# Kernel tuning notes

Hardware: AMD Instinct MI355X
Metric: run time of the kernel (lower is better)

Reference implementation:

```python
import jax, jax.numpy as jnp
import numpy as np

HEADS = 8
HEAD_DIM = 64
INNER = HEADS * HEAD_DIM  # 512
DIM = 512
B, H, W = 8, 32, 32
KV_LEN, KV_DIM = 77, 1024


def group_norm(x, g, b, groups=32, eps=1e-6):
    # x: [B, C, H, W]
    Bx, C, Hx, Wx = x.shape
    xr = x.reshape(Bx, groups, C // groups, Hx, Wx)
    mu = xr.mean(axis=(2, 3, 4), keepdims=True)
    var = xr.var(axis=(2, 3, 4), keepdims=True)
    xr = (xr - mu) * jax.lax.rsqrt(var + eps)
    return xr.reshape(Bx, C, Hx, Wx) * g[None, :, None, None] + b[None, :, None, None]


def layer_norm(x, g, b, eps=1e-5):
    mu = x.mean(axis=-1, keepdims=True)
    var = x.var(axis=-1, keepdims=True)
    return (x - mu) * jax.lax.rsqrt(var + eps) * g + b


def attention(qx, kvx, Wq, Wk, Wv, Wo, bo):
    # qx: [B, Sq, dim_q], kvx: [B, Sk, dim_kv]
    q = qx @ Wq
    k = kvx @ Wk
    v = kvx @ Wv
    Bx, Sq, _ = q.shape
    Sk = k.shape[1]
    q = q.reshape(Bx, Sq, HEADS, HEAD_DIM)
    k = k.reshape(Bx, Sk, HEADS, HEAD_DIM)
    v = v.reshape(Bx, Sk, HEADS, HEAD_DIM)
    att = jnp.einsum('bqhd,bkhd->bhqk', q, k) * (HEAD_DIM ** -0.5)
    att = jax.nn.softmax(att.astype(jnp.float32), axis=-1).astype(q.dtype)
    o = jnp.einsum('bhqk,bkhd->bqhd', att, v).reshape(Bx, Sq, INNER)
    return o @ Wo + bo


def setup_inputs() -> dict:
    key = jax.random.key(0)
    ks = jax.random.split(key, 20)
    s = 0.02
    def n(k, shape):
        return jax.random.normal(k, shape, jnp.float32) * s
    return {
        'q': jax.random.normal(ks[0], (B, DIM, H, W), jnp.float32),
        'kv': jax.random.normal(ks[1], (B, KV_LEN, KV_DIM), jnp.float32),
        'gn_g': jnp.ones((DIM,), jnp.float32), 'gn_b': jnp.zeros((DIM,), jnp.float32),
        'ln2_g': jnp.ones((INNER,), jnp.float32), 'ln2_b': jnp.zeros((INNER,), jnp.float32),
        'ln3_g': jnp.ones((INNER,), jnp.float32), 'ln3_b': jnp.zeros((INNER,), jnp.float32),
        'ln4_g': jnp.ones((INNER,), jnp.float32), 'ln4_b': jnp.zeros((INNER,), jnp.float32),
        'fc_in_w': n(ks[2], (DIM, INNER)), 'fc_in_b': jnp.zeros((INNER,), jnp.float32),
        'fc_out_w': n(ks[3], (INNER, DIM)), 'fc_out_b': jnp.zeros((DIM,), jnp.float32),
        'a1_q': n(ks[4], (INNER, INNER)), 'a1_k': n(ks[5], (INNER, INNER)),
        'a1_v': n(ks[6], (INNER, INNER)), 'a1_o': n(ks[7], (INNER, INNER)),
        'a1_ob': jnp.zeros((INNER,), jnp.float32),
        'a2_q': n(ks[8], (INNER, INNER)), 'a2_k': n(ks[9], (KV_DIM, INNER)),
        'a2_v': n(ks[10], (KV_DIM, INNER)), 'a2_o': n(ks[11], (INNER, INNER)),
        'a2_ob': jnp.zeros((INNER,), jnp.float32),
        'ff_proj_w': n(ks[12], (INNER, INNER * 8)), 'ff_proj_b': jnp.zeros((INNER * 8,), jnp.float32),
        'ff_out_w': n(ks[13], (INNER * 4, INNER)), 'ff_out_b': jnp.zeros((INNER,), jnp.float32),
    }


def reference(q, kv, gn_g, gn_b, ln2_g, ln2_b, ln3_g, ln3_b, ln4_g, ln4_b,
              fc_in_w, fc_in_b, fc_out_w, fc_out_b,
              a1_q, a1_k, a1_v, a1_o, a1_ob,
              a2_q, a2_k, a2_v, a2_o, a2_ob,
              ff_proj_w, ff_proj_b, ff_out_w, ff_out_b):
    res = q
    Bx, C, Hx, Wx = q.shape
    x = group_norm(q, gn_g, gn_b)
    x = x.reshape(Bx, C, Hx * Wx).transpose(0, 2, 1)  # [B, S, C]
    x = x @ fc_in_w + fc_in_b
    t = layer_norm(x, ln2_g, ln2_b)
    x = attention(t, t, a1_q, a1_k, a1_v, a1_o, a1_ob) + x
    x = attention(layer_norm(x, ln3_g, ln3_b), kv, a2_q, a2_k, a2_v, a2_o, a2_ob) + x
    h = layer_norm(x, ln4_g, ln4_b) @ ff_proj_w + ff_proj_b
    a, gate = jnp.split(h, 2, axis=-1)
    x = (a * jax.nn.gelu(gate, approximate=False)) @ ff_out_w + ff_out_b + x
    x = x @ fc_out_w + fc_out_b
    x = x.transpose(0, 2, 1).reshape(Bx, C, Hx, Wx)
    return x + res
```

## Files before the change

### kernel.cpp

```cpp
#include <hip/hip_runtime.h>
#include <cstdint>
#include <cstddef>

typedef __attribute__((ext_vector_type(8))) short bf16x8;
typedef __attribute__((ext_vector_type(4))) short short4v;
typedef __attribute__((ext_vector_type(4))) float f32x4;

__device__ __forceinline__ short f2b(float f) {
    unsigned u = __builtin_bit_cast(unsigned, f);
    u = (u + 0x7FFFu + ((u >> 16) & 1u)) >> 16;
    return (short)u;
}
__device__ __forceinline__ float b2f(short s) {
    unsigned u = ((unsigned)(unsigned short)s) << 16;
    return __builtin_bit_cast(float, u);
}

__device__ __forceinline__ void gload16(const short* g, short* l) {
    __builtin_amdgcn_global_load_lds(
        (const __attribute__((address_space(1))) unsigned int*)g,
        (__attribute__((address_space(3))) unsigned int*)l, 16, 0, 0);
}

__device__ __forceinline__ float gelu_fast(float g) {
    float g2 = g * g;
    float gp = g * (0.7978845608f + 0.0356774081f * g2);
    float e = exp2f(2.885390082f * gp);
    float th = 1.f - 2.f / (e + 1.f);
    return 0.5f * g * (1.f + th);
}

__device__ __forceinline__ int pn_ffp(int n) {
    int m = (n < 2048) ? n : (n - 2048);
    int gofs = (n < 2048) ? 0 : 32;
    int x = m >> 6, c = m & 63;
    return x * 128 + ((c >> 5) << 6) + gofs + (c & 31);
}

struct PrepArgs {
    const float* src[12];
    short* dst[12];
    const float* kv;
    short* kvb;
    const float* fb;
    float* bp;
};

__global__ __launch_bounds__(256) void prep(PrepArgs a) {
    int t = blockIdx.x;
    int tid = threadIdx.x;
    if (t >= 6144) {
        if (t >= 6452) {
            int n = (t - 6452) * 256 + tid;
            if (n < 4096) a.bp[pn_ffp(n)] = a.fb[n];
            return;
        }
        int idx = (t - 6144) * 256 + tid;
        if (idx >= 78848) return;
        const float4* s = (const float4*)a.kv + (size_t)idx * 2;
        float4 va = s[0], vb = s[1];
        bf16x8 w;
        w[0] = f2b(va.x); w[1] = f2b(va.y); w[2] = f2b(va.z); w[3] = f2b(va.w);
        w[4] = f2b(vb.x); w[5] = f2b(vb.y); w[6] = f2b(vb.z); w[7] = f2b(vb.w);
        *(bf16x8*)(a.kvb + (size_t)idx * 8) = w;
        return;
    }
    const int jstart[12] = {0, 256, 512, 768, 1024, 1280, 1536, 1792, 2304, 2816, 3072, 5120};
    const int jK[12] = {512, 512, 512, 512, 512, 512, 512, 1024, 1024, 512, 512, 2048};
    const int jN[12] = {512, 512, 512, 512, 512, 512, 512, 512, 512, 512, 4096, 512};
    int j = 11;
#pragma unroll
    for (int i = 11; i >= 1; --i)
        if (t < jstart[i]) j = i - 1;
    int tx = t - jstart[j];
    int K = jK[j], N = jN[j];
    int tn = N >> 5;
    int n0 = (tx % tn) * 32, k0 = (tx / tn) * 32;
    const float* w = a.src[j];
    short* wt = a.dst[j];
    bool perm = (j == 10);

    __shared__ float tile[32][33];
    int cx = tid & 31, ty0 = tid >> 5;
#pragma unroll
    for (int i = 0; i < 4; ++i) {
        int r = ty0 + i * 8;
        tile[r][cx] = w[(size_t)(k0 + r) * N + n0 + cx];
    }
    __syncthreads();
    int r = tid >> 3;
    int kg = (tid & 7) * 4;
    int drow = perm ? pn_ffp(n0 + r) : (n0 + r);
    short4v o = {f2b(tile[kg][r]), f2b(tile[kg + 1][r]),
                 f2b(tile[kg + 2][r]), f2b(tile[kg + 3][r])};
    *(short4v*)&wt[(size_t)drow * K + k0 + kg] = o;
}

__global__ __launch_bounds__(256) void gn_stats(const float* __restrict__ q,
                                                const float* __restrict__ g,
                                                const float* __restrict__ bta,
                                                float* __restrict__ sc,
                                                float* __restrict__ sh) {
    int bb = blockIdx.x >> 5, gg = blockIdx.x & 31;
    const float4* src = (const float4*)(q + ((size_t)(bb * 512 + gg * 16)) * 1024);
    float s = 0.f, s2 = 0.f;
#pragma unroll
    for (int i = 0; i < 16; ++i) {
        float4 v = src[threadIdx.x + 256 * i];
        s += (v.x + v.y) + (v.z + v.w);
        s2 += (v.x * v.x + v.y * v.y) + (v.z * v.z + v.w * v.w);
    }
#pragma unroll
    for (int m = 1; m < 64; m <<= 1) {
        s += __shfl_xor(s, m);
        s2 += __shfl_xor(s2, m);
    }
    __shared__ float red[8];
    int wv = threadIdx.x >> 6;
    if ((threadIdx.x & 63) == 0) { red[wv] = s; red[4 + wv] = s2; }
    __syncthreads();
    if (threadIdx.x < 16) {
        float S = red[0] + red[1] + red[2] + red[3];
        float S2 = red[4] + red[5] + red[6] + red[7];
        float mu = S * (1.f / 16384.f);
        float var = S2 * (1.f / 16384.f) - mu * mu;
        float rs = rsqrtf(var + 1e-6f);
        int c = gg * 16 + threadIdx.x;
        float scale = rs * g[c];
        sc[bb * 512 + c] = scale;
        sh[bb * 512 + c] = bta[c] - mu * scale;
    }
}

__global__ __launch_bounds__(256) void gn_apply(const float* __restrict__ q,
                                                const float* __restrict__ sc,
                                                const float* __restrict__ sh,
                                                short* __restrict__ out) {
    __shared__ short tile[512][33];
    int b = blockIdx.x >> 5, st = blockIdx.x & 31;
    int s0 = st * 32;
    int sl = threadIdx.x & 31, cg = threadIdx.x >> 5;
    for (int c = cg; c < 512; c += 8) {
        float v = q[((size_t)(b * 512 + c)) * 1024 + s0 + sl];
        float y = v * sc[b * 512 + c] + sh[b * 512 + c];
        tile[c][sl] = f2b(y);
    }
    __syncthreads();
    int sr = threadIdx.x >> 3, ch = threadIdx.x & 7;
    short* orow = out + ((size_t)(b * 1024 + s0 + sr)) * 512;
    for (int c8 = ch * 64; c8 < ch * 64 + 64; c8 += 8) {
        bf16x8 o;
#pragma unroll
        for (int jj = 0; jj < 8; ++jj) o[jj] = tile[c8 + jj][sr];
        *(bf16x8*)&orow[c8] = o;
    }
}

__global__ __launch_bounds__(256) void ln_rows(const short* __restrict__ x,
                                               const float* __restrict__ g,
                                               const float* __restrict__ bta,
                                               short* __restrict__ out) {
    int row = blockIdx.x * 4 + (threadIdx.x >> 6);
    int lane = threadIdx.x & 63;
    bf16x8 v8 = *(const bf16x8*)(x + (size_t)row * 512 + lane * 8);
    float v[8];
#pragma unroll
    for (int j = 0; j < 8; ++j) v[j] = b2f(v8[j]);
    float s = 0.f, s2 = 0.f;
#pragma unroll
    for (int j = 0; j < 8; ++j) { s += v[j]; s2 += v[j] * v[j]; }
#pragma unroll
    for (int m = 1; m < 64; m <<= 1) {
        s += __shfl_xor(s, m);
        s2 += __shfl_xor(s2, m);
    }
    float mu = s * (1.f / 512.f);
    float var = s2 * (1.f / 512.f) - mu * mu;
    float rs = rsqrtf(var + 1e-5f);
    float4 ga = ((const float4*)g)[lane * 2], gb = ((const float4*)g)[lane * 2 + 1];
    float4 ba = ((const float4*)bta)[lane * 2], bb = ((const float4*)bta)[lane * 2 + 1];
    bf16x8 o;
    o[0] = f2b((v[0] - mu) * rs * ga.x + ba.x);
    o[1] = f2b((v[1] - mu) * rs * ga.y + ba.y);
    o[2] = f2b((v[2] - mu) * rs * ga.z + ba.z);
    o[3] = f2b((v[3] - mu) * rs * ga.w + ba.w);
    o[4] = f2b((v[4] - mu) * rs * gb.x + bb.x);
    o[5] = f2b((v[5] - mu) * rs * gb.y + bb.y);
    o[6] = f2b((v[6] - mu) * rs * gb.z + bb.z);
    o[7] = f2b((v[7] - mu) * rs * gb.w + bb.w);
    *(bf16x8*)(out + (size_t)row * 512 + lane * 8) = o;
}

template <int BN>
__global__ __launch_bounds__(256, 1) void gemm_gl(
    const short* __restrict__ A, const short* __restrict__ BT,
    int M, int N, int K,
    const float* __restrict__ bias,
    const short* __restrict__ addSrcB,
    short* __restrict__ outB,
    const float* __restrict__ resid,
    float* __restrict__ outFinal,
    int mode) {
    constexpr int FJ = BN / 32;
    constexpr int ASZ = 3 * 128 * 32;
    constexpr int BSZ = 3 * BN * 32;
    __shared__ __attribute__((aligned(16))) short smem[ASZ + BSZ];
    short* Asb = smem;
    short* Bsb = smem + ASZ;
    int tid = threadIdx.x;
    int wave = tid >> 6, lane = tid & 63;
    int wr = wave >> 1, wc = wave & 1;
    int m0 = blockIdx.y * 128, n0 = blockIdx.x * BN;
    f32x4 acc[4][FJ];
#pragma unroll
    for (int i = 0; i < 4; ++i)
#pragma unroll
        for (int j = 0; j < FJ; ++j) acc[i][j] = (f32x4){0.f, 0.f, 0.f, 0.f};

    int srow = tid >> 2;
    int scg = (((tid & 3) ^ ((tid >> 3) & 3)) << 3);
    int ar0 = m0 + srow; if (ar0 >= M) ar0 = M - 1;
    int ar1 = m0 + 64 + srow; if (ar1 >= M) ar1 = M - 1;
    const short* ag0 = A + (size_t)ar0 * K + scg;
    const short* ag1 = A + (size_t)ar1 * K + scg;
    const short* bg0 = BT + (size_t)(n0 + srow) * K + scg;
    const short* bg1 = BT + (size_t)(n0 + 64 + srow) * K + scg;
    int nk = K >> 5;

    auto stage = [&](int buf) {
        gload16(ag0, &Asb[buf * 4096 + wave * 512]);
        gload16(ag1, &Asb[buf * 4096 + 2048 + wave * 512]);
        gload16(bg0, &Bsb[buf * (BN * 32) + wave * 512]);
        if constexpr (BN == 128) gload16(bg1, &Bsb[buf * 4096 + 2048 + wave * 512]);
        ag0 += 32; ag1 += 32; bg0 += 32; bg1 += 32;
    };
    stage(0);
    stage(1);

    int lr = lane & 15, g = lane >> 4;
    int cur = 0;
    for (int kt = 0; kt < nk; ++kt) {
        __builtin_amdgcn_sched_barrier(0);
        if (kt + 1 < nk) {
            if constexpr (BN == 128) asm volatile("s_waitcnt vmcnt(4)" ::: "memory");
            else asm volatile("s_waitcnt vmcnt(3)" ::: "memory");
        } else {
            asm volatile("s_waitcnt vmcnt(0)" ::: "memory");
        }
        __builtin_amdgcn_sched_barrier(0);
        __builtin_amdgcn_s_barrier();
        int n2 = cur + 2; if (n2 >= 3) n2 -= 3;
        if (kt + 2 < nk) stage(n2);
        bf16x8 af[4], bfr[FJ];
#pragma unroll
        for (int i = 0; i < 4; ++i) {
            int row = wr * 64 + i * 16 + lr;
            af[i] = *(const bf16x8*)&Asb[cur * 4096 + row * 32 + ((g ^ ((row >> 1) & 3)) << 3)];
        }
#pragma unroll
        for (int j = 0; j < FJ; ++j) {
            int row = wc * (BN / 2) + j * 16 + lr;
            bfr[j] = *(const bf16x8*)&Bsb[cur * (BN * 32) + row * 32 + ((g ^ ((row >> 1) & 3)) << 3)];
        }
#pragma unroll
        for (int i = 0; i < 4; ++i)
#pragma unroll
            for (int j = 0; j < FJ; ++j)
                acc[i][j] = __builtin_amdgcn_mfma_f32_16x16x32_bf16(af[i], bfr[j], acc[i][j], 0, 0, 0);
        cur = cur + 1; if (cur >= 3) cur -= 3;
    }

    int lq = lane >> 4;
    if (mode == 1) {
#pragma unroll
        for (int i = 0; i < 4; ++i)
#pragma unroll
            for (int j = 0; j < FJ; ++j) {
                int mm0 = m0 + wr * 64 + i * 16 + lq * 4;
                int nn = n0 + wc * (BN / 2) + j * 16 + lr;
                int bb = mm0 >> 10, ss = mm0 & 1023;
                size_t oi = ((size_t)(bb * 512 + nn)) * 1024 + ss;
                float bv = bias ? bias[nn] : 0.f;
                float4 rv = *(const float4*)&resid[oi];
                float4 ov;
                ov.x = acc[i][j][0] + bv + rv.x;
                ov.y = acc[i][j][1] + bv + rv.y;
                ov.z = acc[i][j][2] + bv + rv.z;
                ov.w = acc[i][j][3] + bv + rv.w;
                *(float4*)&outFinal[oi] = ov;
            }
        return;
    }
    {
        constexpr int EC = BN + 4;
        float* ef = (float*)smem;
#pragma unroll
        for (int h = 0; h < 2; ++h) {
            __syncthreads();
            if (wr == h) {
#pragma unroll
                for (int i = 0; i < 4; ++i)
#pragma unroll
                    for (int j = 0; j < FJ; ++j)
#pragma unroll
                        for (int r = 0; r < 4; ++r)
                            ef[(i * 16 + lq * 4 + r) * EC + wc * (BN / 2) + j * 16 + lr] =
                                acc[i][j][r];
            }
            __syncthreads();
#pragma unroll
            for (int q = 0; q < BN / 16; ++q) {
                int idx = q * 256 + tid;
                int row = idx / (BN / 4);
                int cq = (idx % (BN / 4)) * 4;
                int mm = m0 + h * 64 + row;
                if (mm >= M) continue;
                int nn = n0 + cq;
                float4 v = *(float4*)&ef[row * EC + cq];
                if (bias) {
                    float4 b4 = *(const float4*)&bias[nn];
                    v.x += b4.x; v.y += b4.y; v.z += b4.z; v.w += b4.w;
                }
                size_t ig = (size_t)mm * N + nn;
                if (addSrcB) {
                    short4v a4 = *(const short4v*)&addSrcB[ig];
                    v.x += b2f(a4[0]); v.y += b2f(a4[1]);
                    v.z += b2f(a4[2]); v.w += b2f(a4[3]);
                }
                short4v o = {f2b(v.x), f2b(v.y), f2b(v.z), f2b(v.w)};
                *(short4v*)&outB[ig] = o;
            }
        }
    }
}

__global__ __launch_bounds__(512, 1) void gemm256w(
    const short* __restrict__ A, const short* __restrict__ BT,
    int M, int N, int K,
    const float* __restrict__ bias,
    short* __restrict__ outB,
    int mode) {
    __shared__ __attribute__((aligned(16))) short smem[3 * 4096 + 3 * 8192];
    short* Asb = smem;
    short* Bsb = smem + 12288;
    int tid = threadIdx.x;
    int wave = tid >> 6, lane = tid & 63;
    int wrM = wave >> 2, wcN = wave & 3;
    int m0 = blockIdx.y * 128, n0 = blockIdx.x * 256;
    f32x4 acc[4][4];
#pragma unroll
    for (int i = 0; i < 4; ++i)
#pragma unroll
        for (int j = 0; j < 4; ++j) acc[i][j] = (f32x4){0.f, 0.f, 0.f, 0.f};

    const short* gp[3];
    int ldsoff[3];
    bool isA[3];
#pragma unroll
    for (int s = 0; s < 3; ++s) {
        int qq = wave * 3 + s;
        bool a = qq < 8;
        int r = (a ? qq : qq - 8) * 16 + (lane >> 2);
        int sc = (((lane & 3) ^ ((r >> 1) & 3)) << 3);
        gp[s] = a ? (A + (size_t)(m0 + r) * K + sc)
                  : (BT + (size_t)(n0 + r) * K + sc);
        ldsoff[s] = (a ? qq : (qq - 8)) * 512;
        isA[s] = a;
    }
    int nk = K >> 5;
    auto stage = [&](int buf) {
#pragma unroll
        for (int s = 0; s < 3; ++s) {
            short* l = isA[s] ? &Asb[buf * 4096 + ldsoff[s]]
                              : &Bsb[buf * 8192 + ldsoff[s]];
            gload16(gp[s], l);
            gp[s] += 32;
        }
    };
    stage(0);
    stage(1);

    int lr = lane & 15, g = lane >> 4;
    int cur = 0;
    for (int kt = 0; kt < nk; ++kt) {
        __builtin_amdgcn_sched_barrier(0);
        if (kt + 1 < nk) {
            asm volatile("s_waitcnt vmcnt(3)" ::: "memory");
        } else {
            asm volatile("s_waitcnt vmcnt(0)" ::: "memory");
        }
        __builtin_amdgcn_sched_barrier(0);
        __builtin_amdgcn_s_barrier();
        int n2 = cur + 2; if (n2 >= 3) n2 -= 3;
        if (kt + 2 < nk) stage(n2);
        bf16x8 af[4], bfr[4];
#pragma unroll
        for (int i = 0; i < 4; ++i) {
            int row = wrM * 64 + i * 16 + lr;
            af[i] = *(const bf16x8*)&Asb[cur * 4096 + row * 32 + ((g ^ ((row >> 1) & 3)) << 3)];
        }
#pragma unroll
        for (int j = 0; j < 4; ++j) {
            int row = wcN * 64 + j * 16 + lr;
            bfr[j] = *(const bf16x8*)&Bsb[cur * 8192 + row * 32 + ((g ^ ((row >> 1) & 3)) << 3)];
        }
#pragma unroll
        for (int i = 0; i < 4; ++i)
#pragma unroll
            for (int j = 0; j < 4; ++j)
                acc[i][j] = __builtin_amdgcn_mfma_f32_16x16x32_bf16(af[i], bfr[j], acc[i][j], 0, 0, 0);
        cur = cur + 1; if (cur >= 3) cur -= 3;
    }

    int lq = lane >> 4;
    if (mode == 2) {
        short* eb = smem;
        int xhalf = wcN >> 1, half = wcN & 1;
        __syncthreads();
#pragma unroll
        for (int i = 0; i < 4; ++i)
#pragma unroll
            for (int j = 0; j < 2; ++j)
#pragma unroll
                for (int r = 0; r < 4; ++r) {
                    int slot = n0 + wcN * 64 + j * 16 + lr;
                    float a = acc[i][j][r] + bias[slot];
                    float gt = acc[i][j + 2][r] + bias[slot + 32];
                    float ge = gelu_fast(gt);
                    int row = wrM * 64 + i * 16 + lq * 4 + r;
                    int col = xhalf * 64 + half * 32 + j * 16 + lr;
                    eb[row * 136 + col] = f2b(a * ge);
                }
        __syncthreads();
#pragma unroll
        for (int q = 0; q < 4; ++q) {
            int idx = q * 512 + tid;
            int row = idx >> 4, cg = (idx & 15) * 8;
            bf16x8 o = *(bf16x8*)&eb[row * 136 + cg];
            *(bf16x8*)&outB[(size_t)(m0 + row) * 2048 + blockIdx.x * 128 + cg] = o;
        }
        return;
    }
    {
        float* ef = (float*)smem;
#pragma unroll
        for (int h = 0; h < 2; ++h) {
            __syncthreads();
            if (wrM == h) {
#pragma unroll
                for (int i = 0; i < 4; ++i)
#pragma unroll
                    for (int j = 0; j < 4; ++j)
#pragma unroll
                        for (int r = 0; r < 4; ++r)
                            ef[(i * 16 + lq * 4 + r) * 260 + wcN * 64 + j * 16 + lr] =
                                acc[i][j][r];
            }
            __syncthreads();
#pragma unroll
            for (int q = 0; q < 8; ++q) {
                int idx = q * 512 + tid;
                int row = idx >> 6;
                int cq = (idx & 63) * 4;
                float4 v = *(float4*)&ef[row * 260 + cq];
                int nn = n0 + cq;
                if (bias) {
                    float4 b4 = *(const float4*)&bias[nn];
                    v.x += b4.x; v.y += b4.y; v.z += b4.z; v.w += b4.w;
                }
                short4v o = {f2b(v.x), f2b(v.y), f2b(v.z), f2b(v.w)};
                *(short4v*)&outB[(size_t)(m0 + h * 64 + row) * N + nn] = o;
            }
        }
    }
}

__global__ __launch_bounds__(256, 1) void attn_mfma(const short* __restrict__ qp,
                                                    const short* __restrict__ kp,
                                                    const short* __restrict__ vp,
                                                    short* __restrict__ op,
                                                    int kv_len, int kvBatchRows,
                                                    int qStride, int kvStride) {
    __shared__ __attribute__((aligned(16))) short Kt[64][72];
    __shared__ __attribute__((aligned(16))) short Vt[64][72];
    __shared__ __attribute__((aligned(16))) short Pt[4][2][16][72];
    int tid = threadIdx.x, w = tid >> 6, lane = tid & 63;
    int g = lane >> 4, c = lane & 15;
    int bh = blockIdx.y, b = bh >> 3, h = bh & 7;
    int q0 = blockIdx.x * 128 + w * 16;

    const float QS = 0.125f * 1.44269504f;
    bf16x8 qa[2][2];
#pragma unroll
    for (int qi = 0; qi < 2; ++qi) {
        const short* qbase = qp + ((size_t)(b * 1024 + q0 + qi * 64 + c)) * qStride + h * 64;
        bf16x8 qr0 = *(const bf16x8*)(qbase + g * 8);
        bf16x8 qr1 = *(const bf16x8*)(qbase + 32 + g * 8);
#pragma unroll
        for (int j = 0; j < 8; ++j) {
            qa[qi][0][j] = f2b(b2f(qr0[j]) * QS);
            qa[qi][1][j] = f2b(b2f(qr1[j]) * QS);
        }
    }

    f32x4 oac[2][4];
#pragma unroll
    for (int qi = 0; qi < 2; ++qi)
#pragma unroll
        for (int dt = 0; dt < 4; ++dt) oac[qi][dt] = (f32x4){0.f, 0.f, 0.f, 0.f};
    float l[2][4];
#pragma unroll
    for (int qi = 0; qi < 2; ++qi)
#pragma unroll
        for (int r = 0; r < 4; ++r) l[qi][r] = 0.f;

    int skey = tid & 63, sd0 = (tid >> 6) * 16;
    int ntile = (kv_len + 63) >> 6;
    size_t kvbase = (size_t)b * kvBatchRows;

    bf16x8 k0, k1, v0, v1;
    {
        int krow = skey < kv_len ? skey : kv_len - 1;
        const short* kpp = kp + (kvbase + krow) * kvStride + h * 64 + sd0;
        const short* vpp = vp + (kvbase + krow) * kvStride + h * 64 + sd0;
        k0 = *(const bf16x8*)kpp; k1 = *(const bf16x8*)(kpp + 8);
        v0 = *(const bf16x8*)vpp; v1 = *(const bf16x8*)(vpp + 8);
    }

    for (int kt = 0; kt < ntile; ++kt) {
        __syncthreads();
        *(bf16x8*)&Kt[skey][sd0] = k0;
        *(bf16x8*)&Kt[skey][sd0 + 8] = k1;
#pragma unroll
        for (int j = 0; j < 8; ++j) {
            Vt[sd0 + j][skey] = v0[j];
            Vt[sd0 + 8 + j][skey] = v1[j];
        }
        __syncthreads();
        if (kt + 1 < ntile) {
            int krow = (kt + 1) * 64 + skey;
            if (krow >= kv_len) krow = kv_len - 1;
            const short* kpp = kp + (kvbase + krow) * kvStride + h * 64 + sd0;
            const short* vpp = vp + (kvbase + krow) * kvStride + h * 64 + sd0;
            k0 = *(const bf16x8*)kpp; k1 = *(const bf16x8*)(kpp + 8);
            v0 = *(const bf16x8*)vpp; v1 = *(const bf16x8*)(vpp + 8);
        }

        f32x4 s[2][4];
#pragma unroll
        for (int nt = 0; nt < 4; ++nt) {
            bf16x8 kb0 = *(const bf16x8*)&Kt[nt * 16 + c][g * 8];
            bf16x8 kb1 = *(const bf16x8*)&Kt[nt * 16 + c][32 + g * 8];
#pragma unroll
            for (int qi = 0; qi < 2; ++qi) {
                s[qi][nt] = __builtin_amdgcn_mfma_f32_16x16x32_bf16(
                    qa[qi][0], kb0, (f32x4){0.f, 0.f, 0.f, 0.f}, 0, 0, 0);
                s[qi][nt] = __builtin_amdgcn_mfma_f32_16x16x32_bf16(
                    qa[qi][1], kb1, s[qi][nt], 0, 0, 0);
            }
        }
        if (kt * 64 + 64 > kv_len) {
#pragma unroll
            for (int nt = 0; nt < 4; ++nt) {
                bool valid = kt * 64 + nt * 16 + c < kv_len;
#pragma unroll
                for (int qi = 0; qi < 2; ++qi)
#pragma unroll
                    for (int r = 0; r < 4; ++r) {
                        float pv = valid ? exp2f(s[qi][nt][r]) : 0.f;
                        s[qi][nt][r] = pv;
                        l[qi][r] += pv;
                    }
            }
        } else {
#pragma unroll
            for (int nt = 0; nt < 4; ++nt)
#pragma unroll
                for (int qi = 0; qi < 2; ++qi)
#pragma unroll
                    for (int r = 0; r < 4; ++r) {
                        float pv = exp2f(s[qi][nt][r]);
                        s[qi][nt][r] = pv;
                        l[qi][r] += pv;
                    }
        }

        bf16x8 pa[2][2];
#pragma unroll
        for (int qi = 0; qi < 2; ++qi) {
#pragma unroll
            for (int nt = 0; nt < 4; ++nt)
#pragma unroll
                for (int r = 0; r < 4; ++r)
                    Pt[w][qi][4 * g + r][nt * 16 + c] = f2b(s[qi][nt][r]);
        }
#pragma unroll
        for (int qi = 0; qi < 2; ++qi) {
            pa[qi][0] = *(const bf16x8*)&Pt[w][qi][c][g * 8];
            pa[qi][1] = *(const bf16x8*)&Pt[w][qi][c][32 + g * 8];
        }
#pragma unroll
        for (int dt = 0; dt < 4; ++dt) {
            bf16x8 vb0 = *(const bf16x8*)&Vt[dt * 16 + c][g * 8];
            bf16x8 vb1 = *(const bf16x8*)&Vt[dt * 16 + c][32 + g * 8];
#pragma unroll
            for (int qi = 0; qi < 2; ++qi) {
                oac[qi][dt] = __builtin_amdgcn_mfma_f32_16x16x32_bf16(pa[qi][0], vb0, oac[qi][dt], 0, 0, 0);
                oac[qi][dt] = __builtin_amdgcn_mfma_f32_16x16x32_bf16(pa[qi][1], vb1, oac[qi][dt], 0, 0, 0);
            }
        }
    }

#pragma unroll
    for (int mk = 1; mk < 16; mk <<= 1)
#pragma unroll
        for (int qi = 0; qi < 2; ++qi)
#pragma unroll
            for (int r = 0; r < 4; ++r) l[qi][r] += __shfl_xor(l[qi][r], mk);
#pragma unroll
    for (int qi = 0; qi < 2; ++qi)
#pragma unroll
        for (int r = 0; r < 4; ++r) {
            float inv = 1.f / l[qi][r];
            short* orow = op + ((size_t)(b * 1024 + q0 + qi * 64 + 4 * g + r)) * 512 + h * 64;
#pragma unroll
            for (int dt = 0; dt < 4; ++dt)
                orow[dt * 16 + c] = f2b(oac[qi][dt][r] * inv);
        }
}

extern "C" void kernel_launch(void* const* d_in, const int* in_sizes, int n_in,
                              void* d_out, int out_size, void* d_ws, size_t ws_size,
                              hipStream_t stream) {
    (void)in_sizes; (void)n_in; (void)out_size; (void)ws_size;
    const float* q_in = (const float*)d_in[0];
    const float* kv_in = (const float*)d_in[1];
    const float* gn_g = (const float*)d_in[2];
    const float* gn_b = (const float*)d_in[3];
    const float* ln2_g = (const float*)d_in[4];
    const float* ln2_b = (const float*)d_in[5];
    const float* ln3_g = (const float*)d_in[6];
    const float* ln3_b = (const float*)d_in[7];
    const float* ln4_g = (const float*)d_in[8];
    const float* ln4_b = (const float*)d_in[9];
    const float* fc_in_w = (const float*)d_in[10];
    const float* fc_in_b = (const float*)d_in[11];
    const float* fc_out_w = (const float*)d_in[12];
    const float* fc_out_b = (const float*)d_in[13];
    const float* a1_qw = (const float*)d_in[14];
    const float* a1_kw = (const float*)d_in[15];
    const float* a1_vw = (const float*)d_in[16];
    const float* a1_ow = (const float*)d_in[17];
    const float* a1_ob = (const float*)d_in[18];
    const float* a2_qw = (const float*)d_in[19];
    const float* a2_kw = (const float*)d_in[20];
    const float* a2_vw = (const float*)d_in[21];
    const float* a2_ow = (const float*)d_in[22];
    const float* a2_ob = (const float*)d_in[23];
    const float* ffp_w = (const float*)d_in[24];
    const float* ffp_b = (const float*)d_in[25];
    const float* ffo_w = (const float*)d_in[26];
    const float* ffo_b = (const float*)d_in[27];
    float* out = (float*)d_out;

    char* p = (char*)d_ws;
    auto alloc = [&](size_t n) {
        char* r = p;
        p += (n + 255) & ~(size_t)255;
        return r;
    };
    short* wt_fci = (short*)alloc((size_t)512 * 512 * 2);
    short* wt_fco = (short*)alloc((size_t)512 * 512 * 2);
    short* wt_qkv = (short*)alloc((size_t)1536 * 512 * 2);
    short* wt_a1o = (short*)alloc((size_t)512 * 512 * 2);
    short* wt_a2q = (short*)alloc((size_t)512 * 512 * 2);
    short* wt_kv2 = (short*)alloc((size_t)1024 * 1024 * 2);
    short* wt_a2o = (short*)alloc((size_t)512 * 512 * 2);
    short* wt_ffp = (short*)alloc((size_t)4096 * 512 * 2);
    short* wt_ffo = (short*)alloc((size_t)512 * 2048 * 2);
    float* biasP = (float*)alloc((size_t)4096 * 4);
    short* xb = (short*)alloc((size_t)8192 * 512 * 2);
    short* tb = (short*)alloc((size_t)8192 * 512 * 2);
    short* qkvbuf = (short*)alloc((size_t)8192 * 1536 * 2);
    short* qbuf = (short*)alloc((size_t)8192 * 512 * 2);
    short* kvpbuf = (short*)alloc((size_t)616 * 1024 * 2);
    short* obuf = (short*)alloc((size_t)8192 * 512 * 2);
    short* kvb = (short*)alloc((size_t)616 * 1024 * 2);
    short* ggb = (short*)alloc((size_t)8192 * 2048 * 2);
    float* gnsc = (float*)alloc((size_t)8 * 512 * 4);
    float* gnsh = (float*)alloc((size_t)8 * 512 * 4);

    PrepArgs pa;
    pa.src[0] = fc_in_w;  pa.dst[0] = wt_fci;
    pa.src[1] = fc_out_w; pa.dst[1] = wt_fco;
    pa.src[2] = a1_qw;    pa.dst[2] = wt_qkv;
    pa.src[3] = a1_kw;    pa.dst[3] = wt_qkv + (size_t)512 * 512;
    pa.src[4] = a1_vw;    pa.dst[4] = wt_qkv + (size_t)1024 * 512;
    pa.src[5] = a1_ow;    pa.dst[5] = wt_a1o;
    pa.src[6] = a2_qw;    pa.dst[6] = wt_a2q;
    pa.src[7] = a2_kw;    pa.dst[7] = wt_kv2;
    pa.src[8] = a2_vw;    pa.dst[8] = wt_kv2 + (size_t)512 * 1024;
    pa.src[9] = a2_ow;    pa.dst[9] = wt_a2o;
    pa.src[10] = ffp_w;   pa.dst[10] = wt_ffp;
    pa.src[11] = ffo_w;   pa.dst[11] = wt_ffo;
    pa.kv = kv_in; pa.kvb = kvb; pa.fb = ffp_b; pa.bp = biasP;
    prep<<<6468, 256, 0, stream>>>(pa);

    auto gemm128n = [&](const short* A, const short* BT, int M, int N, int K,
                        const float* bias, const short* addSrcB, short* outB,
                        const float* resid, float* outFinal, int mode) {
        dim3 g(N / 128, (M + 127) / 128);
        gemm_gl<128><<<g, 256, 0, stream>>>(A, BT, M, N, K, bias, addSrcB, outB,
                                            resid, outFinal, mode);
    };
    auto gemm64n = [&](const short* A, const short* BT, int M, int N, int K,
                       const float* bias, const short* addSrcB, short* outB,
                       const float* resid, float* outFinal, int mode) {
        dim3 g(N / 64, (M + 127) / 128);
        gemm_gl<64><<<g, 256, 0, stream>>>(A, BT, M, N, K, bias, addSrcB, outB,
                                           resid, outFinal, mode);
    };

    gn_stats<<<256, 256, 0, stream>>>(q_in, gn_g, gn_b, gnsc, gnsh);
    gn_apply<<<256, 256, 0, stream>>>(q_in, gnsc, gnsh, tb);
    gemm64n(tb, wt_fci, 8192, 512, 512, fc_in_b, nullptr, xb, nullptr, nullptr, 0);
    ln_rows<<<2048, 256, 0, stream>>>(xb, ln2_g, ln2_b, tb);
    gemm256w<<<dim3(6, 64), 512, 0, stream>>>(tb, wt_qkv, 8192, 1536, 512,
                                              nullptr, qkvbuf, 0);
    attn_mfma<<<dim3(8, 64), 256, 0, stream>>>(qkvbuf, qkvbuf + 512, qkvbuf + 1024, obuf,
                                               1024, 1024, 1536, 1536);
    gemm64n(obuf, wt_a1o, 8192, 512, 512, a1_ob, xb, xb, nullptr, nullptr, 0);
    ln_rows<<<2048, 256, 0, stream>>>(xb, ln3_g, ln3_b, tb);
    gemm64n(tb, wt_a2q, 8192, 512, 512, nullptr, nullptr, qbuf, nullptr, nullptr, 0);
    gemm128n(kvb, wt_kv2, 616, 1024, 1024, nullptr, nullptr, kvpbuf, nullptr, nullptr, 0);
    attn_mfma<<<dim3(8, 64), 256, 0, stream>>>(qbuf, kvpbuf, kvpbuf + 512, obuf,
                                               77, 77, 512, 1024);
    gemm64n(obuf, wt_a2o, 8192, 512, 512, a2_ob, xb, xb, nullptr, nullptr, 0);
    ln_rows<<<2048, 256, 0, stream>>>(xb, ln4_g, ln4_b, tb);
    gemm256w<<<dim3(16, 64), 512, 0, stream>>>(tb, wt_ffp, 8192, 4096, 512,
                                               biasP, ggb, 2);
    gemm128n(ggb, wt_ffo, 8192, 512, 2048, ffo_b, xb, tb, nullptr, nullptr, 0);
    gemm64n(tb, wt_fco, 8192, 512, 512, fc_out_b, nullptr, nullptr, q_in, out, 1);
}
```

Measured before the change: 305.9 us.

## Pre-transpose V and triple-buffer K/V tiles via async global-to-LDS loads in attention

Adds a separate kernel that transposes V per head into a contiguous d-major layout, so the attention kernel can stream both K and V tiles with direct global-to-LDS loads instead of register staging and scalar LDS transposes. The attention loop becomes a three-buffer pipeline with explicit vmcnt waits and a single barrier per tile, uses XOR-swizzled LDS addressing to avoid bank conflicts, and raises wave priority around the MFMA blocks. This is meant to hide global load latency and remove the costly per-element V transpose in LDS. In exchange it adds two extra kernel launches and extra memory traffic for the transposed V copies.

```diff
diff --git a/kernel.cpp b/kernel.cpp
--- a/kernel.cpp
+++ b/kernel.cpp
@@ -94,6 +94,34 @@
     short4v o = {f2b(tile[kg][r]), f2b(tile[kg + 1][r]),
                  f2b(tile[kg + 2][r]), f2b(tile[kg + 3][r])};
     *(short4v*)&wt[(size_t)drow * K + k0 + kg] = o;
+}
+
+__global__ __launch_bounds__(256) void vtrans(const short* __restrict__ src,
+                                              short* __restrict__ dst,
+                                              int Svalid, int SrowsPerB,
+                                              int stride, int VS) {
+    __shared__ __attribute__((aligned(16))) short t[64][80];
+    int st = blockIdx.x, bh = blockIdx.y;
+    int b = bh >> 3, h = bh & 7;
+    int s_loc = threadIdx.x >> 2, dg = (threadIdx.x & 3) * 16;
+    int s = st * 64 + s_loc;
+    int sr = s < Svalid ? s : Svalid - 1;
+    const short* p = src + ((size_t)(b * SrowsPerB + sr)) * stride + h * 64 + dg;
+    bf16x8 a0 = *(const bf16x8*)p;
+    bf16x8 a1 = *(const bf16x8*)(p + 8);
+    *(bf16x8*)&t[s_loc][dg] = a0;
+    *(bf16x8*)&t[s_loc][dg + 8] = a1;
+    __syncthreads();
+    int d = threadIdx.x >> 2, sg = (threadIdx.x & 3) * 16;
+    short* q = dst + ((size_t)(bh * 64 + d)) * VS + st * 64 + sg;
+    bf16x8 o0, o1;
+#pragma unroll
+    for (int j = 0; j < 8; ++j) {
+        o0[j] = t[sg + j][d];
+        o1[j] = t[sg + 8 + j][d];
+    }
+    *(bf16x8*)q = o0;
+    *(bf16x8*)(q + 8) = o1;
 }
 
 __global__ __launch_bounds__(256) void gn_stats(const float* __restrict__ q,
@@ -477,12 +505,11 @@
 
 __global__ __launch_bounds__(256, 1) void attn_mfma(const short* __restrict__ qp,
                                                     const short* __restrict__ kp,
-                                                    const short* __restrict__ vp,
+                                                    const short* __restrict__ vtp,
                                                     short* __restrict__ op,
                                                     int kv_len, int kvBatchRows,
-                                                    int qStride, int kvStride) {
-    __shared__ __attribute__((aligned(16))) short Kt[64][72];
-    __shared__ __attribute__((aligned(16))) short Vt[64][72];
+                                                    int qStride, int kStride, int VS) {
+    __shared__ __attribute__((aligned(16))) short KV[3][2][64 * 64];
     __shared__ __attribute__((aligned(16))) short Pt[4][2][16][72];
     int tid = threadIdx.x, w = tid >> 6, lane = tid & 63;
     int g = lane >> 4, c = lane & 15;
@@ -502,6 +529,8 @@
             qa[qi][1][j] = f2b(b2f(qr1[j]) * QS);
         }
     }
+    asm volatile("s_waitcnt vmcnt(0)" ::: "memory");
+    __builtin_amdgcn_sched_barrier(0);
 
     f32x4 oac[2][4];
 #pragma unroll
@@ -514,43 +543,50 @@
 #pragma unroll
         for (int r = 0; r < 4; ++r) l[qi][r] = 0.f;
 
-    int skey = tid & 63, sd0 = (tid >> 6) * 16;
+    int lr8 = lane >> 3, cc = lane & 7;
     int ntile = (kv_len + 63) >> 6;
     size_t kvbase = (size_t)b * kvBatchRows;
-
-    bf16x8 k0, k1, v0, v1;
-    {
-        int krow = skey < kv_len ? skey : kv_len - 1;
-        const short* kpp = kp + (kvbase + krow) * kvStride + h * 64 + sd0;
-        const short* vpp = vp + (kvbase + krow) * kvStride + h * 64 + sd0;
-        k0 = *(const bf16x8*)kpp; k1 = *(const bf16x8*)(kpp + 8);
-        v0 = *(const bf16x8*)vpp; v1 = *(const bf16x8*)(vpp + 8);
-    }
-
+    size_t vtbase = (size_t)bh * 64;
+
+    auto stage = [&](int buf, int kt) {
+#pragma unroll
+        for (int s2 = 0; s2 < 2; ++s2) {
+            int r0 = w * 16 + s2 * 8;
+            int key = kt * 64 + r0 + lr8;
+            if (key >= kv_len) key = kv_len - 1;
+            const short* ksrc = kp + (kvbase + key) * kStride + h * 64 + ((cc ^ lr8) << 3);
+            gload16(ksrc, &KV[buf][0][r0 * 64]);
+            const short* vsrc = vtp + (vtbase + r0 + lr8) * VS + kt * 64 + ((cc ^ lr8) << 3);
+            gload16(vsrc, &KV[buf][1][r0 * 64]);
+        }
+    };
+    stage(0, 0);
+    stage(1, 1);
+
+    int cur = 0;
     for (int kt = 0; kt < ntile; ++kt) {
-        __syncthreads();
-        *(bf16x8*)&Kt[skey][sd0] = k0;
-        *(bf16x8*)&Kt[skey][sd0 + 8] = k1;
-#pragma unroll
-        for (int j = 0; j < 8; ++j) {
-            Vt[sd0 + j][skey] = v0[j];
-            Vt[sd0 + 8 + j][skey] = v1[j];
-        }
-        __syncthreads();
+        __builtin_amdgcn_sched_barrier(0);
         if (kt + 1 < ntile) {
-            int krow = (kt + 1) * 64 + skey;
-            if (krow >= kv_len) krow = kv_len - 1;
-            const short* kpp = kp + (kvbase + krow) * kvStride + h * 64 + sd0;
-            const short* vpp = vp + (kvbase + krow) * kvStride + h * 64 + sd0;
-            k0 = *(const bf16x8*)kpp; k1 = *(const bf16x8*)(kpp + 8);
-            v0 = *(const bf16x8*)vpp; v1 = *(const bf16x8*)(vpp + 8);
-        }
+            asm volatile("s_waitcnt vmcnt(4)" ::: "memory");
+        } else {
+            asm volatile("s_waitcnt vmcnt(0)" ::: "memory");
+        }
+        __builtin_amdgcn_sched_barrier(0);
+        __builtin_amdgcn_s_barrier();
+        int n2 = cur + 2; if (n2 >= 3) n2 -= 3;
+        if (kt + 2 < ntile) stage(n2, kt + 2);
+
+        const short* Kt = &KV[cur][0][0];
+        const short* Vt = &KV[cur][1][0];
+        int c7 = c & 7;
 
         f32x4 s[2][4];
+        __builtin_amdgcn_s_setprio(1);
 #pragma unroll
         for (int nt = 0; nt < 4; ++nt) {
-            bf16x8 kb0 = *(const bf16x8*)&Kt[nt * 16 + c][g * 8];
-            bf16x8 kb1 = *(const bf16x8*)&Kt[nt * 16 + c][32 + g * 8];
+            int row = nt * 16 + c;
+            bf16x8 kb0 = *(const bf16x8*)&Kt[row * 64 + ((g ^ c7) << 3)];
+            bf16x8 kb1 = *(const bf16x8*)&Kt[row * 64 + (((4 + g) ^ c7) << 3)];
 #pragma unroll
             for (int qi = 0; qi < 2; ++qi) {
                 s[qi][nt] = __builtin_amdgcn_mfma_f32_16x16x32_bf16(
@@ -559,6 +595,8 @@
                     qa[qi][1], kb1, s[qi][nt], 0, 0, 0);
             }
         }
+        __builtin_amdgcn_s_setprio(0);
+
         if (kt * 64 + 64 > kv_len) {
 #pragma unroll
             for (int nt = 0; nt < 4; ++nt) {
@@ -599,16 +637,20 @@
             pa[qi][0] = *(const bf16x8*)&Pt[w][qi][c][g * 8];
             pa[qi][1] = *(const bf16x8*)&Pt[w][qi][c][32 + g * 8];
         }
+        __builtin_amdgcn_s_setprio(1);
 #pragma unroll
         for (int dt = 0; dt < 4; ++dt) {
-            bf16x8 vb0 = *(const bf16x8*)&Vt[dt * 16 + c][g * 8];
-            bf16x8 vb1 = *(const bf16x8*)&Vt[dt * 16 + c][32 + g * 8];
+            int row = dt * 16 + c;
+            bf16x8 vb0 = *(const bf16x8*)&Vt[row * 64 + ((g ^ c7) << 3)];
+            bf16x8 vb1 = *(const bf16x8*)&Vt[row * 64 + (((4 + g) ^ c7) << 3)];
 #pragma unroll
             for (int qi = 0; qi < 2; ++qi) {
                 oac[qi][dt] = __builtin_amdgcn_mfma_f32_16x16x32_bf16(pa[qi][0], vb0, oac[qi][dt], 0, 0, 0);
                 oac[qi][dt] = __builtin_amdgcn_mfma_f32_16x16x32_bf16(pa[qi][1], vb1, oac[qi][dt], 0, 0, 0);
             }
         }
+        __builtin_amdgcn_s_setprio(0);
+        cur = cur + 1; if (cur >= 3) cur -= 3;
     }
 
 #pragma unroll
@@ -687,6 +729,8 @@
     short* obuf = (short*)alloc((size_t)8192 * 512 * 2);
     short* kvb = (short*)alloc((size_t)616 * 1024 * 2);
     short* ggb = (short*)alloc((size_t)8192 * 2048 * 2);
+    short* vt1 = (short*)alloc((size_t)64 * 64 * 1024 * 2);
+    short* vt2 = (short*)alloc((size_t)64 * 64 * 128 * 2);
     float* gnsc = (float*)alloc((size_t)8 * 512 * 4);
     float* gnsh = (float*)alloc((size_t)8 * 512 * 4);
 
@@ -727,14 +771,16 @@
     ln_rows<<<2048, 256, 0, stream>>>(xb, ln2_g, ln2_b, tb);
     gemm256w<<<dim3(6, 64), 512, 0, stream>>>(tb, wt_qkv, 8192, 1536, 512,
                                               nullptr, qkvbuf, 0);
-    attn_mfma<<<dim3(8, 64), 256, 0, stream>>>(qkvbuf, qkvbuf + 512, qkvbuf + 1024, obuf,
-                                               1024, 1024, 1536, 1536);
+    vtrans<<<dim3(16, 64), 256, 0, stream>>>(qkvbuf + 1024, vt1, 1024, 1024, 1536, 1024);
+    attn_mfma<<<dim3(8, 64), 256, 0, stream>>>(qkvbuf, qkvbuf + 512, vt1, obuf,
+                                               1024, 1024, 1536, 1536, 1024);
     gemm64n(obuf, wt_a1o, 8192, 512, 512, a1_ob, xb, xb, nullptr, nullptr, 0);
     ln_rows<<<2048, 256, 0, stream>>>(xb, ln3_g, ln3_b, tb);
     gemm64n(tb, wt_a2q, 8192, 512, 512, nullptr, nullptr, qbuf, nullptr, nullptr, 0);
     gemm128n(kvb, wt_kv2, 616, 1024, 1024, nullptr, nullptr, kvpbuf, nullptr, nullptr, 0);
-    attn_mfma<<<dim3(8, 64), 256, 0, stream>>>(qbuf, kvpbuf, kvpbuf + 512, obuf,
-                                               77, 77, 512, 1024);
+    vtrans<<<dim3(2, 64), 256, 0, stream>>>(kvpbuf + 512, vt2, 77, 77, 1024, 128);
+    attn_mfma<<<dim3(8, 64), 256, 0, stream>>>(qbuf, kvpbuf, vt2, obuf,
+                                               77, 77, 512, 1024, 128);
     gemm64n(obuf, wt_a2o, 8192, 512, 512, a2_ob, xb, xb, nullptr, nullptr, 0);
     ln_rows<<<2048, 256, 0, stream>>>(xb, ln4_g, ln4_b, tb);
     gemm256w<<<dim3(16, 64), 512, 0, stream>>>(tb, wt_ffp, 8192, 4096, 512,
```

New measurement: 311.5 us. No clear change (+1.8%).
